# Kernel optimization log

Measured on AMD Instinct MI355X. Metric: run time of the kernel, lower is better.

Reference implementation:

```python
import jax, jax.numpy as jnp
import numpy as np

B, H, L, D = 2, 16, 2048, 64


def setup_inputs() -> dict:
    key = jax.random.key(0)
    kq, kk, kv, km = jax.random.split(key, 4)
    q = jax.random.normal(kq, (B, H, L, D), dtype=jnp.float32)
    k = jax.random.normal(kk, (B, H, L, D), dtype=jnp.float32)
    v = jax.random.normal(kv, (B, H, L, D), dtype=jnp.float32)
    mask = jax.random.uniform(km, (B, L, L), dtype=jnp.float32)
    return {"q": q, "k": k, "v": v, "mask": mask}


def reference(q, k, v, mask):
    d_tensor = k.shape[-1]
    # score = q @ k^T / sqrt(d)  -> [B,H,L,L]
    score = jnp.einsum("bhqd,bhkd->bhqk", q, k) / jnp.sqrt(jnp.float32(d_tensor))
    # multiplicative mask, broadcast over heads (mask: [B,L,L] -> [B,1,L,L])
    score = score * mask[:, None, :, :]
    score = jax.nn.softmax(score, axis=-1)
    out = jnp.einsum("bhqk,bhkd->bhqd", score, v)
    return (out, score)
```

## Files before the change

### kernel.cpp

```cpp
#include <hip/hip_runtime.h>

typedef __attribute__((ext_vector_type(8))) short bf16x8;
typedef __attribute__((ext_vector_type(4))) float f32x4;
typedef __attribute__((ext_vector_type(4))) unsigned u32x4;

#define DEV static __device__ __forceinline__

constexpr int B_ = 2, H_ = 16, L_ = 2048, D_ = 64;
constexpr float SCALE2 = 0.125f * 1.44269504f;

DEV short f2bf(float f) {
  unsigned u = __builtin_bit_cast(unsigned, f);
  u += 0x7fffu + ((u >> 16) & 1u);
  return (short)(u >> 16);
}
DEV unsigned pk2(float lo, float hi) {
  return (unsigned)(unsigned short)f2bf(lo) | ((unsigned)(unsigned short)f2bf(hi) << 16);
}
DEV float bflo(unsigned u) { return __builtin_bit_cast(float, u << 16); }
DEV float bfhi(unsigned u) { return __builtin_bit_cast(float, u & 0xffff0000u); }

DEV bf16x8 frag_from(const float* src) {
  float4 f0 = *(const float4*)src;
  float4 f1 = *(const float4*)(src + 4);
  bf16x8 r;
  r[0] = f2bf(f0.x); r[1] = f2bf(f0.y); r[2] = f2bf(f0.z); r[3] = f2bf(f0.w);
  r[4] = f2bf(f1.x); r[5] = f2bf(f1.y); r[6] = f2bf(f1.z); r[7] = f2bf(f1.w);
  return r;
}

__global__ __launch_bounds__(256) void convert_k_kernel(
    const float* __restrict__ Kg, short* __restrict__ Kp) {
  const int tid = threadIdx.x;
  const int lane = tid & 63, half = (tid >> 6) & 1, sub = tid >> 7;
  const int blk = blockIdx.x;
  const int bh = blk >> 6;
  const int ktile = (((blk & 63) << 1) | sub);
  const int g = lane >> 4, ln = lane & 15;
  const float* src = Kg + ((size_t)bh * L_ + ktile * 16 + ln) * D_ + half * 32 + g * 8;
  bf16x8 f = frag_from(src);
  *(bf16x8*)(Kp + ((size_t)bh * 16384 + ktile * 128 + half * 64 + lane) * 8) = f;
}

__global__ __launch_bounds__(256) void convert_vp_kernel(
    const float* __restrict__ Vg, short* __restrict__ Vp) {
  __shared__ short vt[64 * 256];
  const int tid = threadIdx.x;
  const int bh = blockIdx.x >> 3, c = blockIdx.x & 7;
  const float* vb = Vg + (size_t)bh * L_ * D_ + (size_t)c * 256 * D_;
  const int ka = (tid & 127) * 2, dh = (tid >> 7) * 32;
  const float* r0 = vb + (size_t)ka * D_ + dh;
  const float* r1 = r0 + D_;
#pragma unroll
  for (int i = 0; i < 8; ++i) {
    float4 a = *(const float4*)(r0 + i * 4);
    float4 b = *(const float4*)(r1 + i * 4);
    unsigned p0 = pk2(a.x, b.x), p1 = pk2(a.y, b.y), p2 = pk2(a.z, b.z), p3 = pk2(a.w, b.w);
    const int dd = dh + i * 4;
    *(unsigned*)((char*)vt + (dd + 0) * 512 + ((ka * 2) ^ (((dd + 0) & 7) << 4))) = p0;
    *(unsigned*)((char*)vt + (dd + 1) * 512 + ((ka * 2) ^ (((dd + 1) & 7) << 4))) = p1;
    *(unsigned*)((char*)vt + (dd + 2) * 512 + ((ka * 2) ^ (((dd + 2) & 7) << 4))) = p2;
    *(unsigned*)((char*)vt + (dd + 3) * 512 + ((ka * 2) ^ (((dd + 3) & 7) << 4))) = p3;
  }
  __syncthreads();
  u32x4* out = (u32x4*)Vp + (size_t)(bh * 8 + c) * 2048;
#pragma unroll
  for (int i = 0; i < 8; ++i) {
    const int u = tid + 256 * i;
    const int lane = u & 63, w = (u >> 6) & 7, n = u >> 9;
    const int g = lane >> 4, ln = lane & 15;
    const int d = n * 16 + ln;
    const int kb = (w * 32 + g * 4) * 2;
    const char* rowp = (const char*)vt + d * 512;
    const int swz = (d & 7) << 4;
    uint2 lo = *(const uint2*)(rowp + (kb ^ swz));
    uint2 hi = *(const uint2*)(rowp + ((kb + 32) ^ swz));
    out[u] = u32x4{lo.x, lo.y, hi.x, hi.y};
  }
}

template <bool USEPRE>
__global__ __launch_bounds__(512, 4) void attn_fused(
    const float* __restrict__ Qg, const float* __restrict__ Kg,
    const short* __restrict__ Kp, const float* __restrict__ Vg,
    const short* __restrict__ Vpg, const float* __restrict__ Mg,
    float* __restrict__ Pg, float* __restrict__ Og) {
  const int tid = threadIdx.x;
  const int w = tid >> 6, lane = tid & 63;
  const int g = lane >> 4, ln = lane & 15;

  const int bid = blockIdx.x;
  const int wg = (bid & 7) * 512 + (bid >> 3);
  const int q0 = (wg & 127) << 4;
  const int bh = wg >> 7;
  const int b = bh >> 4;

  __shared__ u32x4 vstage[2][2048];
  __shared__ float red[8][16];

  const float* qp = Qg + (size_t)bh * L_ * D_;
  const float* mrow = Mg + (size_t)b * L_ * L_ + (size_t)(q0 + ln) * L_;
  float* prow = Pg + (size_t)bh * L_ * L_ + (size_t)(q0 + ln) * L_;

  bf16x8 qf0 = frag_from(qp + (size_t)(q0 + ln) * D_ + g * 8);
  bf16x8 qf1 = frag_from(qp + (size_t)(q0 + ln) * D_ + 32 + g * 8);

  unsigned pkv[32];
  float mx = -1e30f;
  const bf16x8* kb_ = (const bf16x8*)Kp + (size_t)bh * 16384 + lane;

#define TILE_OF(j) (2 * w + (((j) >> 1) << 4) + ((j) & 1))

  bf16x8 k0c, k1c, k0n, k1n;
  float4 mkc, mkn;
  {
    const int t0 = TILE_OF(0);
    if (USEPRE) {
      k0c = kb_[t0 * 128];
      k1c = kb_[t0 * 128 + 64];
    } else {
      const float* kr = Kg + (size_t)bh * L_ * D_ + (size_t)(t0 * 16 + ln) * D_;
      k0c = frag_from(kr + g * 8);
      k1c = frag_from(kr + 32 + g * 8);
    }
    mkc = *(const float4*)(mrow + t0 * 16 + g * 4);
  }
#pragma unroll
  for (int j = 0; j < 16; ++j) {
    if (j < 15) {
      const int tn = TILE_OF(j + 1);
      if (USEPRE) {
        k0n = kb_[tn * 128];
        k1n = kb_[tn * 128 + 64];
      } else {
        const float* kr = Kg + (size_t)bh * L_ * D_ + (size_t)(tn * 16 + ln) * D_;
        k0n = frag_from(kr + g * 8);
        k1n = frag_from(kr + 32 + g * 8);
      }
      mkn = *(const float4*)(mrow + tn * 16 + g * 4);
    }
    f32x4 acc{0.f, 0.f, 0.f, 0.f};
    acc = __builtin_amdgcn_mfma_f32_16x16x32_bf16(k0c, qf0, acc, 0, 0, 0);
    acc = __builtin_amdgcn_mfma_f32_16x16x32_bf16(k1c, qf1, acc, 0, 0, 0);
    float l0 = acc[0] * SCALE2 * mkc.x;
    float l1 = acc[1] * SCALE2 * mkc.y;
    float l2 = acc[2] * SCALE2 * mkc.z;
    float l3 = acc[3] * SCALE2 * mkc.w;
    mx = fmaxf(mx, fmaxf(fmaxf(l0, l1), fmaxf(l2, l3)));
    pkv[2 * j] = pk2(l0, l1);
    pkv[2 * j + 1] = pk2(l2, l3);
    k0c = k0n; k1c = k1n; mkc = mkn;
  }

  const u32x4* vp4 = (const u32x4*)Vpg + (size_t)bh * 8 * 2048;
  u32x4 sv0, sv1, sv2, sv3;
  if (USEPRE) {
    sv0 = vp4[0 * 512 + tid];
    sv1 = vp4[1 * 512 + tid];
    sv2 = vp4[2 * 512 + tid];
    sv3 = vp4[3 * 512 + tid];
  }

  mx = fmaxf(mx, __shfl_xor(mx, 16));
  mx = fmaxf(mx, __shfl_xor(mx, 32));
  if (lane < 16) red[w][ln] = mx;
  __syncthreads();
  {
    float t = red[0][ln];
#pragma unroll
    for (int ww = 1; ww < 8; ++ww) t = fmaxf(t, red[ww][ln]);
    mx = t;
  }
  float sm = 0.f;
#pragma unroll
  for (int j = 0; j < 16; ++j) {
    float e0 = exp2f(bflo(pkv[2 * j]) - mx);
    float e1 = exp2f(bfhi(pkv[2 * j]) - mx);
    float e2 = exp2f(bflo(pkv[2 * j + 1]) - mx);
    float e3 = exp2f(bfhi(pkv[2 * j + 1]) - mx);
    sm += (e0 + e1) + (e2 + e3);
    pkv[2 * j] = pk2(e0, e1);
    pkv[2 * j + 1] = pk2(e2, e3);
  }
  sm += __shfl_xor(sm, 16);
  sm += __shfl_xor(sm, 32);
  __syncthreads();
  if (lane < 16) red[w][ln] = sm;
  if (USEPRE) {
    vstage[0][0 * 512 + tid] = sv0;
    vstage[0][1 * 512 + tid] = sv1;
    vstage[0][2 * 512 + tid] = sv2;
    vstage[0][3 * 512 + tid] = sv3;
  }
  __syncthreads();
  float inv;
  {
    float t = red[0][ln];
#pragma unroll
    for (int ww = 1; ww < 8; ++ww) t += red[ww][ln];
    inv = 1.0f / t;
  }

  f32x4 acc_o[4];
#pragma unroll
  for (int n = 0; n < 4; ++n) acc_o[n] = f32x4{0.f, 0.f, 0.f, 0.f};

  const float* vsrc_f32 = Vg + (size_t)bh * L_ * D_;

#pragma unroll
  for (int c = 0; c < 8; ++c) {
    if (USEPRE && c < 7) {
      sv0 = vp4[(size_t)(c + 1) * 2048 + 0 * 512 + tid];
      sv1 = vp4[(size_t)(c + 1) * 2048 + 1 * 512 + tid];
      sv2 = vp4[(size_t)(c + 1) * 2048 + 2 * 512 + tid];
      sv3 = vp4[(size_t)(c + 1) * 2048 + 3 * 512 + tid];
    }
    unsigned u0 = pkv[4 * c], u1 = pkv[4 * c + 1], u2 = pkv[4 * c + 2], u3 = pkv[4 * c + 3];
    float n0 = bflo(u0) * inv, n1 = bfhi(u0) * inv;
    float n2 = bflo(u1) * inv, n3 = bfhi(u1) * inv;
    float n4 = bflo(u2) * inv, n5 = bfhi(u2) * inv;
    float n6 = bflo(u3) * inv, n7 = bfhi(u3) * inv;
    const int te = 2 * w + 16 * c;
    f32x4 s0{n0, n1, n2, n3};
    f32x4 s1{n4, n5, n6, n7};
    __builtin_nontemporal_store(s0, (f32x4*)(prow + te * 16 + g * 4));
    __builtin_nontemporal_store(s1, (f32x4*)(prow + (te + 1) * 16 + g * 4));
    u32x4 au{pk2(n0, n1), pk2(n2, n3), pk2(n4, n5), pk2(n6, n7)};
    bf16x8 pa = __builtin_bit_cast(bf16x8, au);
#pragma unroll
    for (int n = 0; n < 4; ++n) {
      bf16x8 bf;
      if (USEPRE) {
        bf = __builtin_bit_cast(bf16x8, vstage[c & 1][(n * 8 + w) * 64 + lane]);
      } else {
        const int k0i = c * 256 + w * 32 + g * 4;
        const int d = n * 16 + ln;
        const float* vbp = vsrc_f32 + d;
#pragma unroll
        for (int e = 0; e < 4; ++e) bf[e] = f2bf(vbp[(size_t)(k0i + e) * D_]);
#pragma unroll
        for (int e = 0; e < 4; ++e) bf[4 + e] = f2bf(vbp[(size_t)(k0i + 16 + e) * D_]);
      }
      acc_o[n] = __builtin_amdgcn_mfma_f32_16x16x32_bf16(pa, bf, acc_o[n], 0, 0, 0);
    }
    if (USEPRE && c < 7) {
      vstage[(c + 1) & 1][0 * 512 + tid] = sv0;
      vstage[(c + 1) & 1][1 * 512 + tid] = sv1;
      vstage[(c + 1) & 1][2 * 512 + tid] = sv2;
      vstage[(c + 1) & 1][3 * 512 + tid] = sv3;
    }
    __syncthreads();
  }

  float* red_o = (float*)&vstage[0][0];
#pragma unroll
  for (int n = 0; n < 4; ++n)
#pragma unroll
    for (int r = 0; r < 4; ++r)
      red_o[(w * 16 + g * 4 + r) * 64 + n * 16 + ln] = acc_o[n][r];
  __syncthreads();
  {
    float* ob = Og + (size_t)bh * L_ * D_ + (size_t)q0 * D_;
    const int row = tid >> 5, dp = (tid & 31) * 2;
    float s0 = 0.f, s1 = 0.f;
#pragma unroll
    for (int ww = 0; ww < 8; ++ww) {
      s0 += red_o[(ww * 16 + row) * 64 + dp];
      s1 += red_o[(ww * 16 + row) * 64 + dp + 1];
    }
    __builtin_nontemporal_store(s0, ob + row * D_ + dp);
    __builtin_nontemporal_store(s1, ob + row * D_ + dp + 1);
  }
}

extern "C" void kernel_launch(void* const* d_in, const int* in_sizes, int n_in,
                              void* d_out, int out_size, void* d_ws, size_t ws_size,
                              hipStream_t stream) {
  const float* q = (const float*)d_in[0];
  const float* k = (const float*)d_in[1];
  const float* v = (const float*)d_in[2];
  const float* mask = (const float*)d_in[3];
  float* out = (float*)d_out;
  float* score = out + (size_t)B_ * H_ * L_ * D_;

  const size_t elems = (size_t)B_ * H_ * L_ * D_;
  const size_t need = elems * 2 * sizeof(short);
  const int nblk = B_ * H_ * (L_ / 16);

  if (ws_size >= need) {
    short* kp = (short*)d_ws;
    short* vp = kp + elems;
    convert_k_kernel<<<2048, 256, 0, stream>>>(k, kp);
    convert_vp_kernel<<<B_ * H_ * 8, 256, 0, stream>>>(v, vp);
    attn_fused<true><<<nblk, 512, 0, stream>>>(q, k, kp, v, vp, mask, score, out);
  } else {
    attn_fused<false><<<nblk, 512, 0, stream>>>(q, k, nullptr, v, nullptr, mask, score, out);
  }
}
```

Baseline: 238.9 us.

## Load V fragments straight to registers and remap blocks head-fastest for mask reuse

The shared-memory double buffer for V is replaced by per-thread register prefetch two chunks ahead, which removes the LDS writes and the barrier inside the PV loop and halves the shared-memory footprint. Block indexing is also remapped so that consecutive work items vary the head first. Blocks reading the same mask rows (same batch and query tile) then run close together and can hit in L2. The cost is more live registers for the prefetched V fragments, and with fewer barriers the waves of a block can drift apart.

```diff
diff --git a/kernel.cpp b/kernel.cpp
--- a/kernel.cpp
+++ b/kernel.cpp
@@ -91,11 +91,13 @@
 
   const int bid = blockIdx.x;
   const int wg = (bid & 7) * 512 + (bid >> 3);
-  const int q0 = (wg & 127) << 4;
-  const int bh = wg >> 7;
-  const int b = bh >> 4;
-
-  __shared__ u32x4 vstage[2][2048];
+  const int h = wg & 15;
+  const int qt = (wg >> 4) & 127;
+  const int b = wg >> 11;
+  const int bh = b * 16 + h;
+  const int q0 = qt << 4;
+
+  __shared__ float red_o[128 * 64];
   __shared__ float red[8][16];
 
   const float* qp = Qg + (size_t)bh * L_ * D_;
@@ -153,12 +155,16 @@
   }
 
   const u32x4* vp4 = (const u32x4*)Vpg + (size_t)bh * 8 * 2048;
-  u32x4 sv0, sv1, sv2, sv3;
+  u32x4 vcur0, vcur1, vcur2, vcur3, vnxt0, vnxt1, vnxt2, vnxt3;
   if (USEPRE) {
-    sv0 = vp4[0 * 512 + tid];
-    sv1 = vp4[1 * 512 + tid];
-    sv2 = vp4[2 * 512 + tid];
-    sv3 = vp4[3 * 512 + tid];
+    vcur0 = vp4[0 * 512 + tid];
+    vcur1 = vp4[1 * 512 + tid];
+    vcur2 = vp4[2 * 512 + tid];
+    vcur3 = vp4[3 * 512 + tid];
+    vnxt0 = vp4[2048 + 0 * 512 + tid];
+    vnxt1 = vp4[2048 + 1 * 512 + tid];
+    vnxt2 = vp4[2048 + 2 * 512 + tid];
+    vnxt3 = vp4[2048 + 3 * 512 + tid];
   }
 
   mx = fmaxf(mx, __shfl_xor(mx, 16));
@@ -186,12 +192,6 @@
   sm += __shfl_xor(sm, 32);
   __syncthreads();
   if (lane < 16) red[w][ln] = sm;
-  if (USEPRE) {
-    vstage[0][0 * 512 + tid] = sv0;
-    vstage[0][1 * 512 + tid] = sv1;
-    vstage[0][2 * 512 + tid] = sv2;
-    vstage[0][3 * 512 + tid] = sv3;
-  }
   __syncthreads();
   float inv;
   {
@@ -209,11 +209,29 @@
 
 #pragma unroll
   for (int c = 0; c < 8; ++c) {
-    if (USEPRE && c < 7) {
-      sv0 = vp4[(size_t)(c + 1) * 2048 + 0 * 512 + tid];
-      sv1 = vp4[(size_t)(c + 1) * 2048 + 1 * 512 + tid];
-      sv2 = vp4[(size_t)(c + 1) * 2048 + 2 * 512 + tid];
-      sv3 = vp4[(size_t)(c + 1) * 2048 + 3 * 512 + tid];
+    u32x4 b0 = vcur0, b1 = vcur1, b2 = vcur2, b3 = vcur3;
+    if (USEPRE) {
+      vcur0 = vnxt0; vcur1 = vnxt1; vcur2 = vnxt2; vcur3 = vnxt3;
+      if (c < 6) {
+        vnxt0 = vp4[(size_t)(c + 2) * 2048 + 0 * 512 + tid];
+        vnxt1 = vp4[(size_t)(c + 2) * 2048 + 1 * 512 + tid];
+        vnxt2 = vp4[(size_t)(c + 2) * 2048 + 2 * 512 + tid];
+        vnxt3 = vp4[(size_t)(c + 2) * 2048 + 3 * 512 + tid];
+      }
+    } else {
+      const int k0i = c * 256 + w * 32 + g * 4;
+#pragma unroll
+      for (int n = 0; n < 4; ++n) {
+        const int d = n * 16 + ln;
+        const float* vbp = vsrc_f32 + d;
+        bf16x8 bf;
+#pragma unroll
+        for (int e = 0; e < 4; ++e) bf[e] = f2bf(vbp[(size_t)(k0i + e) * D_]);
+#pragma unroll
+        for (int e = 0; e < 4; ++e) bf[4 + e] = f2bf(vbp[(size_t)(k0i + 16 + e) * D_]);
+        u32x4 bu = __builtin_bit_cast(u32x4, bf);
+        if (n == 0) b0 = bu; else if (n == 1) b1 = bu; else if (n == 2) b2 = bu; else b3 = bu;
+      }
     }
     unsigned u0 = pkv[4 * c], u1 = pkv[4 * c + 1], u2 = pkv[4 * c + 2], u3 = pkv[4 * c + 3];
     float n0 = bflo(u0) * inv, n1 = bfhi(u0) * inv;
@@ -227,32 +245,12 @@
     __builtin_nontemporal_store(s1, (f32x4*)(prow + (te + 1) * 16 + g * 4));
     u32x4 au{pk2(n0, n1), pk2(n2, n3), pk2(n4, n5), pk2(n6, n7)};
     bf16x8 pa = __builtin_bit_cast(bf16x8, au);
-#pragma unroll
-    for (int n = 0; n < 4; ++n) {
-      bf16x8 bf;
-      if (USEPRE) {
-        bf = __builtin_bit_cast(bf16x8, vstage[c & 1][(n * 8 + w) * 64 + lane]);
-      } else {
-        const int k0i = c * 256 + w * 32 + g * 4;
-        const int d = n * 16 + ln;
-        const float* vbp = vsrc_f32 + d;
-#pragma unroll
-        for (int e = 0; e < 4; ++e) bf[e] = f2bf(vbp[(size_t)(k0i + e) * D_]);
-#pragma unroll
-        for (int e = 0; e < 4; ++e) bf[4 + e] = f2bf(vbp[(size_t)(k0i + 16 + e) * D_]);
-      }
-      acc_o[n] = __builtin_amdgcn_mfma_f32_16x16x32_bf16(pa, bf, acc_o[n], 0, 0, 0);
-    }
-    if (USEPRE && c < 7) {
-      vstage[(c + 1) & 1][0 * 512 + tid] = sv0;
-      vstage[(c + 1) & 1][1 * 512 + tid] = sv1;
-      vstage[(c + 1) & 1][2 * 512 + tid] = sv2;
-      vstage[(c + 1) & 1][3 * 512 + tid] = sv3;
-    }
-    __syncthreads();
-  }
-
-  float* red_o = (float*)&vstage[0][0];
+    acc_o[0] = __builtin_amdgcn_mfma_f32_16x16x32_bf16(pa, __builtin_bit_cast(bf16x8, b0), acc_o[0], 0, 0, 0);
+    acc_o[1] = __builtin_amdgcn_mfma_f32_16x16x32_bf16(pa, __builtin_bit_cast(bf16x8, b1), acc_o[1], 0, 0, 0);
+    acc_o[2] = __builtin_amdgcn_mfma_f32_16x16x32_bf16(pa, __builtin_bit_cast(bf16x8, b2), acc_o[2], 0, 0, 0);
+    acc_o[3] = __builtin_amdgcn_mfma_f32_16x16x32_bf16(pa, __builtin_bit_cast(bf16x8, b3), acc_o[3], 0, 0, 0);
+  }
+
 #pragma unroll
   for (int n = 0; n < 4; ++n)
 #pragma unroll
```

New measurement: 352.0 us. 1.47x slower.
